# Kernel tuning notes

Measured on AMD Instinct MI355X. Metric: run time of the kernel, lower is better.

The kernel has to match this reference:

```python
import jax, jax.numpy as jnp
import numpy as np

N_LIG, N_TGT, E = 100000, 20000, 250000
LIG_IN, TGT_IN, H = 4, 1280, 128


def setup_inputs() -> dict:
    key = jax.random.key(0)
    ks = jax.random.split(key, 12)
    def lin_w(k, fan_in, fan_out):
        # kaiming-uniform-ish init, stored as [in, out] for x @ W
        bound = 1.0 / np.sqrt(fan_in)
        return jax.random.uniform(k, (fan_in, fan_out), jnp.float32, -bound, bound)
    return {
        "x_ligand": jax.random.normal(ks[0], (N_LIG, LIG_IN), jnp.float32),
        "x_target": jax.random.normal(ks[1], (N_TGT, TGT_IN), jnp.float32),
        "edge_src": jax.random.randint(ks[2], (E,), 0, N_LIG, jnp.int32),
        "edge_dst": jax.random.randint(ks[3], (E,), 0, N_TGT, jnp.int32),
        # SAGEConv (ligand -> target): lin_l on aggregated ligand msgs, lin_r on target self
        "W_lt_l": lin_w(ks[4], LIG_IN, H),
        "b_lt_l": jnp.zeros((H,), jnp.float32),
        "W_lt_r": lin_w(ks[5], TGT_IN, H),
        # SAGEConv (target -> ligand): lin_l on aggregated target msgs, lin_r on ligand self
        "W_tl_l": lin_w(ks[6], TGT_IN, H),
        "b_tl_l": jnp.zeros((H,), jnp.float32),
        "W_tl_r": lin_w(ks[7], LIG_IN, H),
        # edge predictor: Linear(2H -> 1)
        "W_ep": lin_w(ks[8], 2 * H, 1),
        "b_ep": jnp.zeros((1,), jnp.float32),
    }


def _mean_agg(x_src, src_idx, dst_idx, num_dst):
    # gather per-edge source features, scatter-mean onto destination nodes
    msg = x_src[src_idx]                                             # [E, F]
    s = jax.ops.segment_sum(msg, dst_idx, num_segments=num_dst)      # [N_dst, F]
    cnt = jax.ops.segment_sum(jnp.ones((src_idx.shape[0], 1), x_src.dtype),
                              dst_idx, num_segments=num_dst)         # [N_dst, 1]
    return s / jnp.maximum(cnt, 1.0)


def reference(x_ligand, x_target, edge_src, edge_dst,
              W_lt_l, b_lt_l, W_lt_r, W_tl_l, b_tl_l, W_tl_r, W_ep, b_ep):
    # SAGEConv (ligand, binds_to, target): aggregate ligand msgs into targets
    agg_t = _mean_agg(x_ligand, edge_src, edge_dst, N_TGT)           # [N_TGT, LIG_IN]
    t_out = agg_t @ W_lt_l + b_lt_l + x_target @ W_lt_r              # [N_TGT, H]
    # SAGEConv (target, binds_to, ligand): reversed edges (flip(0))
    agg_l = _mean_agg(x_target, edge_dst, edge_src, N_LIG)           # [N_LIG, TGT_IN]
    l_out = agg_l @ W_tl_l + b_tl_l + x_ligand @ W_tl_r              # [N_LIG, H]
    l_out = jax.nn.relu(l_out)
    t_out = jax.nn.relu(t_out)
    # edge predictor: gather endpoints, concat, linear, squeeze
    edge_feats = jnp.concatenate([l_out[edge_src], t_out[edge_dst]], axis=-1)  # [E, 2H]
    out = (edge_feats @ W_ep + b_ep).squeeze(-1)                     # [E]
    return out
```

## Files before the change

kernel.cpp:

```cpp
#include <hip/hip_runtime.h>
#include <hip/hip_bf16.h>


#define H 128
#define K_DIM 1280
#define LIG_IN 4
#define CAP_L 24
#define CAP_T 48

typedef __attribute__((ext_vector_type(8))) short bf16x8;
typedef __attribute__((ext_vector_type(4))) float f32x4;

#define AS1(p) ((const __attribute__((address_space(1))) void*)(p))
#define AS3(p) ((__attribute__((address_space(3))) void*)(p))

__global__ void fill_both(const int* __restrict__ src, const int* __restrict__ dst,
                          int* __restrict__ cur_l, int* __restrict__ cur_t,
                          int* __restrict__ adjd, int* __restrict__ adjs, int E)
{
    int e = blockIdx.x * blockDim.x + threadIdx.x;
    if (e >= E) return;
    int s = src[e], d = dst[e];
    int p = atomicAdd(&cur_l[s], 1);
    adjd[s * CAP_L + p] = d;
    int q = atomicAdd(&cur_t[d], 1);
    adjs[d * CAP_T + q] = s;
}

__global__ void cast_x(const float4* __restrict__ in, uint4* __restrict__ out, int n8)
{
    int i = blockIdx.x * blockDim.x + threadIdx.x;
    if (i >= n8) return;
    float4 v0 = in[i * 2], v1 = in[i * 2 + 1];
    union { __hip_bfloat16 h[8]; uint4 u; } r;
    r.h[0] = __float2bfloat16(v0.x); r.h[1] = __float2bfloat16(v0.y);
    r.h[2] = __float2bfloat16(v0.z); r.h[3] = __float2bfloat16(v0.w);
    r.h[4] = __float2bfloat16(v1.x); r.h[5] = __float2bfloat16(v1.y);
    r.h[6] = __float2bfloat16(v1.z); r.h[7] = __float2bfloat16(v1.w);
    out[i] = r.u;
}

__global__ void cast_wt(const float* __restrict__ Wl, const float* __restrict__ Wr,
                        __hip_bfloat16* __restrict__ Wt, int n)
{
    int idx = blockIdx.x * blockDim.x + threadIdx.x;
    if (idx >= n) return;
    int nr = idx / K_DIM, k = idx - nr * K_DIM;
    float v = (nr < H) ? Wl[k * H + nr] : Wr[k * H + (nr - H)];
    Wt[idx] = __float2bfloat16(v);
}

__global__ __launch_bounds__(256)
void gemm_mfma(const unsigned short* __restrict__ Xb,
               const unsigned short* __restrict__ Wt,
               float* __restrict__ y_tl, float* __restrict__ t_lin, int M)
{
    __shared__ short As[128 * 32];
    __shared__ short Bs[128 * 32];

    const int mb = blockIdx.x >> 1, nb = blockIdx.x & 1;
    const int bm = mb * 128;
    const int w = threadIdx.x >> 6, lane = threadIdx.x & 63;
    const int wm = w & 1, wn = w >> 1;
    float* __restrict__ Y = nb ? t_lin : y_tl;

    const int qa = w * 128 + lane;
    const int q0 = qa, q1 = qa + 64;
    const int r0 = min(bm + (q0 >> 2), M - 1), c0 = q0 & 3;
    const int r1 = min(bm + (q1 >> 2), M - 1), c1 = q1 & 3;
    const int bn128 = nb * 128;
    const int rb0 = bn128 + (q0 >> 2), cb0 = c0;
    const int rb1 = bn128 + (q1 >> 2), cb1 = c1;

    const unsigned short* gA0 = Xb + (size_t)r0 * K_DIM + c0 * 8;
    const unsigned short* gA1 = Xb + (size_t)r1 * K_DIM + c1 * 8;
    const unsigned short* gB0 = Wt + (size_t)rb0 * K_DIM + cb0 * 8;
    const unsigned short* gB1 = Wt + (size_t)rb1 * K_DIM + cb1 * 8;

    char* lA0 = (char*)As + (w * 2 + 0) * 1024;
    char* lA1 = (char*)As + (w * 2 + 1) * 1024;
    char* lB0 = (char*)Bs + (w * 2 + 0) * 1024;
    char* lB1 = (char*)Bs + (w * 2 + 1) * 1024;

    f32x4 acc[4][4];
#pragma unroll
    for (int i = 0; i < 4; ++i)
#pragma unroll
        for (int j = 0; j < 4; ++j)
            acc[i][j] = (f32x4){0.f, 0.f, 0.f, 0.f};

    const int mrow = lane & 15, q = lane >> 4;

    for (int k0 = 0; k0 < K_DIM; k0 += 32) {
        __builtin_amdgcn_global_load_lds(AS1(gA0 + k0), AS3(lA0), 16, 0, 0);
        __builtin_amdgcn_global_load_lds(AS1(gA1 + k0), AS3(lA1), 16, 0, 0);
        __builtin_amdgcn_global_load_lds(AS1(gB0 + k0), AS3(lB0), 16, 0, 0);
        __builtin_amdgcn_global_load_lds(AS1(gB1 + k0), AS3(lB1), 16, 0, 0);
        __syncthreads();

        bf16x8 aF[4], bF[4];
#pragma unroll
        for (int i = 0; i < 4; ++i)
            aF[i] = *(const bf16x8*)((const char*)As + (wm * 64 + i * 16 + mrow) * 64 + q * 16);
#pragma unroll
        for (int j = 0; j < 4; ++j)
            bF[j] = *(const bf16x8*)((const char*)Bs + (wn * 64 + j * 16 + mrow) * 64 + q * 16);
#pragma unroll
        for (int i = 0; i < 4; ++i)
#pragma unroll
            for (int j = 0; j < 4; ++j)
                acc[i][j] = __builtin_amdgcn_mfma_f32_16x16x32_bf16(aF[i], bF[j], acc[i][j], 0, 0, 0);
        __syncthreads();
    }

#pragma unroll
    for (int i = 0; i < 4; ++i) {
#pragma unroll
        for (int r = 0; r < 4; ++r) {
            int row = bm + wm * 64 + i * 16 + (lane >> 4) * 4 + r;
            if (row < M) {
#pragma unroll
                for (int j = 0; j < 4; ++j) {
                    int col = wn * 64 + j * 16 + (lane & 15);
                    Y[(size_t)row * H + col] = acc[i][j][r];
                }
            }
        }
    }
}

__global__ void target_post(const int* __restrict__ cur_t, const int* __restrict__ adjs,
                            const float* __restrict__ xl, const float* __restrict__ t_lin,
                            const float* __restrict__ W_lt_l, const float* __restrict__ b_lt_l,
                            const float* __restrict__ W_ep,
                            float* __restrict__ st, int NT)
{
    int wid = (blockIdx.x * blockDim.x + threadIdx.x) >> 6;
    int lane = threadIdx.x & 63;
    if (wid >= NT) return;
    int cnt = cur_t[wid];
    float a0 = 0.f, a1 = 0.f, a2 = 0.f, a3 = 0.f;
    for (int j = lane; j < cnt; j += 64) {
        int s = adjs[wid * CAP_T + j];
        float4 v = *(const float4*)(xl + (size_t)s * LIG_IN);
        a0 += v.x; a1 += v.y; a2 += v.z; a3 += v.w;
    }
#pragma unroll
    for (int off = 32; off > 0; off >>= 1) {
        a0 += __shfl_xor(a0, off);
        a1 += __shfl_xor(a1, off);
        a2 += __shfl_xor(a2, off);
        a3 += __shfl_xor(a3, off);
    }
    float inv = 1.0f / fmaxf((float)cnt, 1.0f);
    a0 *= inv; a1 *= inv; a2 *= inv; a3 *= inv;
    float acc = 0.f;
#pragma unroll
    for (int p = 0; p < 2; ++p) {
        int h = lane + p * 64;
        float v = a0 * W_lt_l[h] + a1 * W_lt_l[H + h] + a2 * W_lt_l[2 * H + h] +
                  a3 * W_lt_l[3 * H + h] + b_lt_l[h] + t_lin[(size_t)wid * H + h];
        v = fmaxf(v, 0.f);
        acc += v * W_ep[H + h];
    }
#pragma unroll
    for (int off = 32; off > 0; off >>= 1) acc += __shfl_down(acc, off);
    if (lane == 0) st[wid] = acc;
}

__global__ void ligand_gather_post(const int* __restrict__ cur_l, const int* __restrict__ adjd,
                                   const float* __restrict__ y_tl,
                                   const float* __restrict__ xl,
                                   const float* __restrict__ W_tl_r, const float* __restrict__ b_tl_l,
                                   const float* __restrict__ W_ep,
                                   float* __restrict__ sl, int NL)
{
    int wid = (blockIdx.x * blockDim.x + threadIdx.x) >> 6;
    int lane = threadIdx.x & 63;
    if (wid >= NL) return;
    int cnt = cur_l[wid];
    float a0 = 0.f, a1 = 0.f;
    for (int j = 0; j < cnt; ++j) {
        int d = adjd[wid * CAP_L + j];
        const float* row = y_tl + (size_t)d * H;
        a0 += row[lane];
        a1 += row[lane + 64];
    }
    float inv = 1.0f / fmaxf((float)cnt, 1.0f);
    float4 x = *(const float4*)(xl + (size_t)wid * LIG_IN);
    float acc = 0.f;
    {
        int h = lane;
        float v = a0 * inv + b_tl_l[h] +
                  x.x * W_tl_r[h] + x.y * W_tl_r[H + h] +
                  x.z * W_tl_r[2 * H + h] + x.w * W_tl_r[3 * H + h];
        v = fmaxf(v, 0.f);
        acc += v * W_ep[h];
    }
    {
        int h = lane + 64;
        float v = a1 * inv + b_tl_l[h] +
                  x.x * W_tl_r[h] + x.y * W_tl_r[H + h] +
                  x.z * W_tl_r[2 * H + h] + x.w * W_tl_r[3 * H + h];
        v = fmaxf(v, 0.f);
        acc += v * W_ep[h];
    }
#pragma unroll
    for (int off = 32; off > 0; off >>= 1) acc += __shfl_down(acc, off);
    if (lane == 0) sl[wid] = acc;
}

__global__ void edge_out(const int* __restrict__ src, const int* __restrict__ dst,
                         const float* __restrict__ sl, const float* __restrict__ st,
                         const float* __restrict__ b_ep, float* __restrict__ out, int E)
{
    int e = blockIdx.x * blockDim.x + threadIdx.x;
    if (e >= E) return;
    out[e] = sl[src[e]] + st[dst[e]] + b_ep[0];
}

extern "C" void kernel_launch(void* const* d_in, const int* in_sizes, int n_in,
                              void* d_out, int out_size, void* d_ws, size_t ws_size,
                              hipStream_t stream) {
    const float* x_ligand = (const float*)d_in[0];
    const float* x_target = (const float*)d_in[1];
    const int*   edge_src = (const int*)d_in[2];
    const int*   edge_dst = (const int*)d_in[3];
    const float* W_lt_l   = (const float*)d_in[4];
    const float* b_lt_l   = (const float*)d_in[5];
    const float* W_lt_r   = (const float*)d_in[6];
    const float* W_tl_l   = (const float*)d_in[7];
    const float* b_tl_l   = (const float*)d_in[8];
    const float* W_tl_r   = (const float*)d_in[9];
    const float* W_ep     = (const float*)d_in[10];
    const float* b_ep     = (const float*)d_in[11];
    float* out = (float*)d_out;

    const int NL = in_sizes[0] / LIG_IN;
    const int NT = in_sizes[1] / K_DIM;
    const int E  = in_sizes[2];

    char* ws = (char*)d_ws;
    size_t off = 0;
    auto take = [&](size_t bytes) { size_t o = off; off += (bytes + 15) & ~(size_t)15; return o; };
    size_t off_Xb     = take((size_t)NT * K_DIM * 2);
    size_t off_Wt     = take((size_t)2 * H * K_DIM * 2);
    size_t off_y_tl   = take((size_t)NT * H * 4);
    size_t off_t_lin  = take((size_t)NT * H * 4);
    size_t off_adjd   = take((size_t)NL * CAP_L * 4);
    size_t off_adjs   = take((size_t)NT * CAP_T * 4);
    size_t off_cur_l  = take((size_t)NL * 4);
    size_t off_cur_t  = take((size_t)NT * 4);
    size_t off_sl     = take((size_t)NL * 4);
    size_t off_st     = take((size_t)NT * 4);
    if (off > ws_size) {
        hipMemsetAsync(d_out, 0, (size_t)out_size * 4, stream);
        return;
    }

    unsigned short* Xb = (unsigned short*)(ws + off_Xb);
    __hip_bfloat16* Wt = (__hip_bfloat16*)(ws + off_Wt);
    float* y_tl  = (float*)(ws + off_y_tl);
    float* t_lin = (float*)(ws + off_t_lin);
    int*   adjd  = (int*)(ws + off_adjd);
    int*   adjs  = (int*)(ws + off_adjs);
    int*   cur_l = (int*)(ws + off_cur_l);
    int*   cur_t = (int*)(ws + off_cur_t);
    float* sl    = (float*)(ws + off_sl);
    float* st    = (float*)(ws + off_st);

    hipMemsetAsync(cur_l, 0, off_sl - off_cur_l, stream);

    fill_both<<<(E + 255) / 256, 256, 0, stream>>>(edge_src, edge_dst,
                                                   cur_l, cur_t, adjd, adjs, E);
    int n8 = NT * K_DIM / 8;
    cast_x<<<(n8 + 255) / 256, 256, 0, stream>>>((const float4*)x_target, (uint4*)Xb, n8);
    int nw = 2 * H * K_DIM;
    cast_wt<<<(nw + 255) / 256, 256, 0, stream>>>(W_tl_l, W_lt_r, Wt, nw);

    int nMB = (NT + 127) / 128;
    gemm_mfma<<<nMB * 2, 256, 0, stream>>>(Xb, (const unsigned short*)Wt, y_tl, t_lin, NT);

    target_post<<<(NT * 64 + 255) / 256, 256, 0, stream>>>(cur_t, adjs, x_ligand, t_lin,
                                                           W_lt_l, b_lt_l, W_ep, st, NT);
    ligand_gather_post<<<(NL * 64 + 255) / 256, 256, 0, stream>>>(cur_l, adjd, y_tl, x_ligand,
                                                                  W_tl_r, b_tl_l, W_ep, sl, NL);
    edge_out<<<(E + 255) / 256, 256, 0, stream>>>(edge_src, edge_dst, sl, st, b_ep, out, E);
}
```

Measured before the change: 310.4 us.

## Fuse fp32-to-bf16 cast of x_target into GEMM and retile to 64x256

Drops the separate cast_x kernel and its bf16 staging buffer. The GEMM now reads fp32 x_target directly, converts each slice to bf16 in registers and writes it to LDS. Tiles are reshaped so each block covers 64 rows by the full 256 output columns (both weight halves), which means x_target is read exactly once rather than once per N-half. The cost is an A-load that goes through registers instead of the direct global-to-LDS path, and fewer blocks (313) running the same total work.

```diff
diff --git a/kernel.cpp b/kernel.cpp
--- a/kernel.cpp
+++ b/kernel.cpp
@@ -27,19 +27,6 @@
     adjs[d * CAP_T + q] = s;
 }
 
-__global__ void cast_x(const float4* __restrict__ in, uint4* __restrict__ out, int n8)
-{
-    int i = blockIdx.x * blockDim.x + threadIdx.x;
-    if (i >= n8) return;
-    float4 v0 = in[i * 2], v1 = in[i * 2 + 1];
-    union { __hip_bfloat16 h[8]; uint4 u; } r;
-    r.h[0] = __float2bfloat16(v0.x); r.h[1] = __float2bfloat16(v0.y);
-    r.h[2] = __float2bfloat16(v0.z); r.h[3] = __float2bfloat16(v0.w);
-    r.h[4] = __float2bfloat16(v1.x); r.h[5] = __float2bfloat16(v1.y);
-    r.h[6] = __float2bfloat16(v1.z); r.h[7] = __float2bfloat16(v1.w);
-    out[i] = r.u;
-}
-
 __global__ void cast_wt(const float* __restrict__ Wl, const float* __restrict__ Wr,
                         __hip_bfloat16* __restrict__ Wt, int n)
 {
@@ -51,36 +38,32 @@
 }
 
 __global__ __launch_bounds__(256)
-void gemm_mfma(const unsigned short* __restrict__ Xb,
-               const unsigned short* __restrict__ Wt,
-               float* __restrict__ y_tl, float* __restrict__ t_lin, int M)
-{
-    __shared__ short As[128 * 32];
-    __shared__ short Bs[128 * 32];
-
-    const int mb = blockIdx.x >> 1, nb = blockIdx.x & 1;
-    const int bm = mb * 128;
+void gemm_fused(const float* __restrict__ Xf,
+                const unsigned short* __restrict__ Wt,
+                float* __restrict__ y_tl, float* __restrict__ t_lin, int M)
+{
+    __shared__ short As[64 * 32];
+    __shared__ short Bs[256 * 32];
+
+    const int bm = blockIdx.x * 64;
     const int w = threadIdx.x >> 6, lane = threadIdx.x & 63;
-    const int wm = w & 1, wn = w >> 1;
-    float* __restrict__ Y = nb ? t_lin : y_tl;
-
-    const int qa = w * 128 + lane;
-    const int q0 = qa, q1 = qa + 64;
-    const int r0 = min(bm + (q0 >> 2), M - 1), c0 = q0 & 3;
-    const int r1 = min(bm + (q1 >> 2), M - 1), c1 = q1 & 3;
-    const int bn128 = nb * 128;
-    const int rb0 = bn128 + (q0 >> 2), cb0 = c0;
-    const int rb1 = bn128 + (q1 >> 2), cb1 = c1;
-
-    const unsigned short* gA0 = Xb + (size_t)r0 * K_DIM + c0 * 8;
-    const unsigned short* gA1 = Xb + (size_t)r1 * K_DIM + c1 * 8;
-    const unsigned short* gB0 = Wt + (size_t)rb0 * K_DIM + cb0 * 8;
-    const unsigned short* gB1 = Wt + (size_t)rb1 * K_DIM + cb1 * 8;
-
-    char* lA0 = (char*)As + (w * 2 + 0) * 1024;
-    char* lA1 = (char*)As + (w * 2 + 1) * 1024;
-    char* lB0 = (char*)Bs + (w * 2 + 0) * 1024;
-    char* lB1 = (char*)Bs + (w * 2 + 1) * 1024;
+    const int mrow = lane & 15, quad = lane >> 4;
+
+    const int a_row = threadIdx.x >> 2;
+    const int a_seg = threadIdx.x & 3;
+    const float* gA = Xf + (size_t)min(bm + a_row, M - 1) * K_DIM + a_seg * 8;
+    char* lA = (char*)As + a_row * 64 + a_seg * 16;
+
+    const unsigned short* gB[4];
+    char* lB[4];
+#pragma unroll
+    for (int i = 0; i < 4; ++i) {
+        int q = i * 64 + lane;
+        int row = w * 64 + (q >> 2);
+        int seg = q & 3;
+        gB[i] = Wt + (size_t)row * K_DIM + seg * 8;
+        lB[i] = (char*)Bs + w * 4096 + i * 1024 + lane * 16;
+    }
 
     f32x4 acc[4][4];
 #pragma unroll
@@ -89,22 +72,27 @@
         for (int j = 0; j < 4; ++j)
             acc[i][j] = (f32x4){0.f, 0.f, 0.f, 0.f};
 
-    const int mrow = lane & 15, q = lane >> 4;
-
     for (int k0 = 0; k0 < K_DIM; k0 += 32) {
-        __builtin_amdgcn_global_load_lds(AS1(gA0 + k0), AS3(lA0), 16, 0, 0);
-        __builtin_amdgcn_global_load_lds(AS1(gA1 + k0), AS3(lA1), 16, 0, 0);
-        __builtin_amdgcn_global_load_lds(AS1(gB0 + k0), AS3(lB0), 16, 0, 0);
-        __builtin_amdgcn_global_load_lds(AS1(gB1 + k0), AS3(lB1), 16, 0, 0);
+#pragma unroll
+        for (int i = 0; i < 4; ++i)
+            __builtin_amdgcn_global_load_lds(AS1(gB[i] + k0), AS3(lB[i]), 16, 0, 0);
+        float4 v0 = *(const float4*)(gA + k0);
+        float4 v1 = *(const float4*)(gA + k0 + 4);
+        union { __hip_bfloat16 h[8]; uint4 u; } r;
+        r.h[0] = __float2bfloat16(v0.x); r.h[1] = __float2bfloat16(v0.y);
+        r.h[2] = __float2bfloat16(v0.z); r.h[3] = __float2bfloat16(v0.w);
+        r.h[4] = __float2bfloat16(v1.x); r.h[5] = __float2bfloat16(v1.y);
+        r.h[6] = __float2bfloat16(v1.z); r.h[7] = __float2bfloat16(v1.w);
+        *(uint4*)lA = r.u;
         __syncthreads();
 
         bf16x8 aF[4], bF[4];
 #pragma unroll
         for (int i = 0; i < 4; ++i)
-            aF[i] = *(const bf16x8*)((const char*)As + (wm * 64 + i * 16 + mrow) * 64 + q * 16);
+            aF[i] = *(const bf16x8*)((const char*)As + (i * 16 + mrow) * 64 + quad * 16);
 #pragma unroll
         for (int j = 0; j < 4; ++j)
-            bF[j] = *(const bf16x8*)((const char*)Bs + (wn * 64 + j * 16 + mrow) * 64 + q * 16);
+            bF[j] = *(const bf16x8*)((const char*)Bs + (w * 64 + j * 16 + mrow) * 64 + quad * 16);
 #pragma unroll
         for (int i = 0; i < 4; ++i)
 #pragma unroll
@@ -113,15 +101,17 @@
         __syncthreads();
     }
 
+    float* __restrict__ Y = (w < 2) ? y_tl : t_lin;
+    const int cbase = (w & 1) * 64;
 #pragma unroll
     for (int i = 0; i < 4; ++i) {
 #pragma unroll
         for (int r = 0; r < 4; ++r) {
-            int row = bm + wm * 64 + i * 16 + (lane >> 4) * 4 + r;
+            int row = bm + i * 16 + quad * 4 + r;
             if (row < M) {
 #pragma unroll
                 for (int j = 0; j < 4; ++j) {
-                    int col = wn * 64 + j * 16 + (lane & 15);
+                    int col = cbase + j * 16 + mrow;
                     Y[(size_t)row * H + col] = acc[i][j][r];
                 }
             }
@@ -243,7 +233,6 @@
     char* ws = (char*)d_ws;
     size_t off = 0;
     auto take = [&](size_t bytes) { size_t o = off; off += (bytes + 15) & ~(size_t)15; return o; };
-    size_t off_Xb     = take((size_t)NT * K_DIM * 2);
     size_t off_Wt     = take((size_t)2 * H * K_DIM * 2);
     size_t off_y_tl   = take((size_t)NT * H * 4);
     size_t off_t_lin  = take((size_t)NT * H * 4);
@@ -258,7 +247,6 @@
         return;
     }
 
-    unsigned short* Xb = (unsigned short*)(ws + off_Xb);
     __hip_bfloat16* Wt = (__hip_bfloat16*)(ws + off_Wt);
     float* y_tl  = (float*)(ws + off_y_tl);
     float* t_lin = (float*)(ws + off_t_lin);
@@ -273,13 +261,11 @@
 
     fill_both<<<(E + 255) / 256, 256, 0, stream>>>(edge_src, edge_dst,
                                                    cur_l, cur_t, adjd, adjs, E);
-    int n8 = NT * K_DIM / 8;
-    cast_x<<<(n8 + 255) / 256, 256, 0, stream>>>((const float4*)x_target, (uint4*)Xb, n8);
     int nw = 2 * H * K_DIM;
     cast_wt<<<(nw + 255) / 256, 256, 0, stream>>>(W_tl_l, W_lt_r, Wt, nw);
 
-    int nMB = (NT + 127) / 128;
-    gemm_mfma<<<nMB * 2, 256, 0, stream>>>(Xb, (const unsigned short*)Wt, y_tl, t_lin, NT);
+    int nMB = (NT + 63) / 64;
+    gemm_fused<<<nMB, 256, 0, stream>>>(x_target, (const unsigned short*)Wt, y_tl, t_lin, NT);
 
     target_post<<<(NT * 64 + 255) / 256, 256, 0, stream>>>(cur_t, adjs, x_ligand, t_lin,
                                                            W_lt_l, b_lt_l, W_ep, st, NT);
```

New measurement: 310.7 us. About the same (+0.1%).
